# Optimization experiments

Hardware: AMD Instinct MI355X
Metric: run time of the kernel (lower is better)

## Reference

```python
import jax, jax.numpy as jnp
import numpy as np
import itertools

MAX_SRC_PER_MIX = 2
N_OUT = 2 * MAX_SRC_PER_MIX          # 4 estimated sources
N_COMB = 2 ** N_OUT                  # 16 assignment combinations
SNR_MAX = 30.0


def _a_tensor():
    # [16, 2, 4]: row 0 = combination mask, row 1 = its complement
    combos = np.array(list(itertools.product([0, 1], repeat=N_OUT)), dtype=np.float32)
    return jnp.asarray(np.stack([combos, 1.0 - combos], axis=1))


def setup_inputs() -> dict:
    key = jax.random.key(0)
    k1, k2, k3 = jax.random.split(key, 3)
    B, T = 32, 64000
    return {
        "estimated_sources": jax.random.normal(k1, (B, N_OUT, T), dtype=jnp.float32),
        "m1": jax.random.normal(k2, (B, T), dtype=jnp.float32),
        "m2": jax.random.normal(k3, (B, T), dtype=jnp.float32),
    }


def _snr_loss(y, y_pred):
    # y: [K, B, T] estimated mixture, y_pred: [1, B, T] reference mixture
    a = jnp.sum((y - y_pred) ** 2, axis=-1)   # [K, B]
    b = jnp.sum(y ** 2, axis=-1)              # [K, B]
    loss = 10.0 * jnp.log10(a + SNR_MAX * b) - 10.0 * jnp.log10(b)
    return jnp.sum(loss, axis=-1)             # [K]


def reference(estimated_sources, m1, m2):
    A = _a_tensor()                                              # [K, 2, S]
    # all combinations x batch in one contraction (contraction dim S=4)
    mix = jnp.einsum('kcs,bst->kbct', A, estimated_sources)      # [K, B, 2, T]
    losses = _snr_loss(mix[:, :, 0], m1[None]) + _snr_loss(mix[:, :, 1], m2[None])  # [K]
    return jnp.argmin(losses), jnp.min(losses)
```

## Files before the change

### kernel.cpp

```cpp
#include <hip/hip_runtime.h>
#include <math.h>

#define B      32
#define NSRC   4
#define T      64000
#define CH     16
#define NACC   20
#define KCOMB  16
#define TLEN4  ((T / CH) / 4)


__global__ __launch_bounds__(256) void mixit_reduce_kernel(
    const float* __restrict__ est, const float* __restrict__ m1,
    const float* __restrict__ m2, float* __restrict__ ws)
{
    const int b  = blockIdx.x / CH;
    const int ch = blockIdx.x % CH;

    const float4* e0 = (const float4*)(est + (size_t)b * NSRC * T) + (size_t)ch * TLEN4;
    const float4* e1 = e0 + T / 4;
    const float4* e2 = e1 + T / 4;
    const float4* e3 = e2 + T / 4;
    const float4* p1 = (const float4*)(m1 + (size_t)b * T) + (size_t)ch * TLEN4;
    const float4* p2 = (const float4*)(m2 + (size_t)b * T) + (size_t)ch * TLEN4;

    float acc[NACC];
#pragma unroll
    for (int i = 0; i < NACC; i++) acc[i] = 0.0f;

    for (int i = threadIdx.x; i < TLEN4; i += 256) {
        float4 v0 = e0[i], v1 = e1[i], v2 = e2[i], v3 = e3[i];
        float4 w1 = p1[i], w2 = p2[i];
        float A0[4] = {v0.x, v0.y, v0.z, v0.w};
        float A1[4] = {v1.x, v1.y, v1.z, v1.w};
        float A2[4] = {v2.x, v2.y, v2.z, v2.w};
        float A3[4] = {v3.x, v3.y, v3.z, v3.w};
        float M1[4] = {w1.x, w1.y, w1.z, w1.w};
        float M2[4] = {w2.x, w2.y, w2.z, w2.w};
#pragma unroll
        for (int j = 0; j < 4; j++) {
            float s0 = A0[j], s1 = A1[j], s2 = A2[j], s3 = A3[j];
            float x = M1[j], y = M2[j];
            acc[0]  = fmaf(s0, s0, acc[0]);
            acc[1]  = fmaf(s0, s1, acc[1]);
            acc[2]  = fmaf(s0, s2, acc[2]);
            acc[3]  = fmaf(s0, s3, acc[3]);
            acc[4]  = fmaf(s1, s1, acc[4]);
            acc[5]  = fmaf(s1, s2, acc[5]);
            acc[6]  = fmaf(s1, s3, acc[6]);
            acc[7]  = fmaf(s2, s2, acc[7]);
            acc[8]  = fmaf(s2, s3, acc[8]);
            acc[9]  = fmaf(s3, s3, acc[9]);
            acc[10] = fmaf(s0, x,  acc[10]);
            acc[11] = fmaf(s1, x,  acc[11]);
            acc[12] = fmaf(s2, x,  acc[12]);
            acc[13] = fmaf(s3, x,  acc[13]);
            acc[14] = fmaf(s0, y,  acc[14]);
            acc[15] = fmaf(s1, y,  acc[15]);
            acc[16] = fmaf(s2, y,  acc[16]);
            acc[17] = fmaf(s3, y,  acc[17]);
            acc[18] = fmaf(x,  x,  acc[18]);
            acc[19] = fmaf(y,  y,  acc[19]);
        }
    }

#pragma unroll
    for (int i = 0; i < NACC; i++) {
        float v = acc[i];
#pragma unroll
        for (int off = 32; off >= 1; off >>= 1) v += __shfl_xor(v, off, 64);
        acc[i] = v;
    }

    __shared__ float lds[4][NACC];
    const int lane = threadIdx.x & 63;
    const int wave = threadIdx.x >> 6;
    if (lane == 0) {
#pragma unroll
        for (int i = 0; i < NACC; i++) lds[wave][i] = acc[i];
    }
    __syncthreads();
    if (threadIdx.x < NACC) {
        float s = lds[0][threadIdx.x] + lds[1][threadIdx.x] +
                  lds[2][threadIdx.x] + lds[3][threadIdx.x];
        ws[(size_t)blockIdx.x * NACC + threadIdx.x] = s;
    }
}

__global__ __launch_bounds__(256) void mixit_finalize_kernel(
    const float* __restrict__ ws, float* __restrict__ out)
{
    __shared__ float sums[B * NACC];
    __shared__ float losses[KCOMB];

    for (int p = threadIdx.x; p < B * NACC; p += 256) {
        int b = p / NACC, i = p % NACC;
        float s = 0.0f;
        for (int ch = 0; ch < CH; ch++)
            s += ws[(size_t)(b * CH + ch) * NACC + i];
        sums[p] = s;
    }
    __syncthreads();

    if (threadIdx.x < KCOMB) {
        const int k = threadIdx.x;
        float m0 = (float)((k >> 3) & 1);
        float m1b = (float)((k >> 2) & 1);
        float m2b = (float)((k >> 1) & 1);
        float m3 = (float)(k & 1);
        float u0 = 1.0f - m0, u1 = 1.0f - m1b, u2 = 1.0f - m2b, u3 = 1.0f - m3;

        float loss = 0.0f;
        for (int b = 0; b < B; b++) {
            const float* a = sums + b * NACC;
            float g00 = a[0], g01 = a[1], g02 = a[2], g03 = a[3];
            float g11 = a[4], g12 = a[5], g13 = a[6];
            float g22 = a[7], g23 = a[8], g33 = a[9];

            float q0 = m0*m0*g00 + m1b*m1b*g11 + m2b*m2b*g22 + m3*m3*g33
                     + 2.0f*(m0*m1b*g01 + m0*m2b*g02 + m0*m3*g03
                           + m1b*m2b*g12 + m1b*m3*g13 + m2b*m3*g23);
            float q1 = u0*u0*g00 + u1*u1*g11 + u2*u2*g22 + u3*u3*g33
                     + 2.0f*(u0*u1*g01 + u0*u2*g02 + u0*u3*g03
                           + u1*u2*g12 + u1*u3*g13 + u2*u3*g23);
            float d1 = m0*a[10] + m1b*a[11] + m2b*a[12] + m3*a[13];
            float d2 = u0*a[14] + u1*a[15] + u2*a[16] + u3*a[17];
            float n1 = a[18], n2 = a[19];

            float a0 = q0 - 2.0f*d1 + n1;
            float a1 = q1 - 2.0f*d2 + n2;

            loss += 10.0f * (log10f(fmaf(30.0f, q0, a0)) - log10f(q0));
            loss += 10.0f * (log10f(fmaf(30.0f, q1, a1)) - log10f(q1));
        }
        losses[k] = loss;
    }
    __syncthreads();

    if (threadIdx.x == 0) {
        float best = losses[0];
        int bi = 0;
        for (int k = 1; k < KCOMB; k++) {
            if (losses[k] < best) { best = losses[k]; bi = k; }
        }
        out[0] = (float)bi;
        out[1] = best;
    }
}

extern "C" void kernel_launch(void* const* d_in, const int* in_sizes, int n_in,
                              void* d_out, int out_size, void* d_ws, size_t ws_size,
                              hipStream_t stream) {
    const float* est = (const float*)d_in[0];
    const float* m1  = (const float*)d_in[1];
    const float* m2  = (const float*)d_in[2];
    float* ws  = (float*)d_ws;
    float* out = (float*)d_out;

    mixit_reduce_kernel<<<B * CH, 256, 0, stream>>>(est, m1, m2, ws);
    mixit_finalize_kernel<<<1, 256, 0, stream>>>(ws, out);
}
```

Before: 96.59 us.

## Fuse reduce and finalize via last-block atomic counter, add prefetch and DPP reductions

```diff
diff --git a/kernel.cpp b/kernel.cpp
--- a/kernel.cpp
+++ b/kernel.cpp
@@ -7,15 +7,66 @@
 #define CH     16
 #define NACC   20
 #define KCOMB  16
+#define NBLK   (B * CH)
 #define TLEN4  ((T / CH) / 4)
-
-
-__global__ __launch_bounds__(256) void mixit_reduce_kernel(
+#define CNT_BYTE_OFF (NBLK * NACC * 4)
+
+#define DPP_QX1   0xB1
+#define DPP_QX2   0x4E
+#define DPP_HMIRR 0x141
+#define DPP_MIRR  0x140
+
+template <int CTRL>
+__device__ __forceinline__ float dpp_add(float v) {
+    int x = __builtin_amdgcn_update_dpp(0, __float_as_int(v), CTRL, 0xF, 0xF, true);
+    return v + __int_as_float(x);
+}
+
+__device__ __forceinline__ void accum20(float* __restrict__ acc,
+        const float4 v0, const float4 v1, const float4 v2, const float4 v3,
+        const float4 w1, const float4 w2)
+{
+    const float A0[4] = {v0.x, v0.y, v0.z, v0.w};
+    const float A1[4] = {v1.x, v1.y, v1.z, v1.w};
+    const float A2[4] = {v2.x, v2.y, v2.z, v2.w};
+    const float A3[4] = {v3.x, v3.y, v3.z, v3.w};
+    const float M1[4] = {w1.x, w1.y, w1.z, w1.w};
+    const float M2[4] = {w2.x, w2.y, w2.z, w2.w};
+#pragma unroll
+    for (int j = 0; j < 4; j++) {
+        float s0 = A0[j], s1 = A1[j], s2 = A2[j], s3 = A3[j];
+        float x = M1[j], y = M2[j];
+        acc[0]  = fmaf(s0, s0, acc[0]);
+        acc[1]  = fmaf(s0, s1, acc[1]);
+        acc[2]  = fmaf(s0, s2, acc[2]);
+        acc[3]  = fmaf(s0, s3, acc[3]);
+        acc[4]  = fmaf(s1, s1, acc[4]);
+        acc[5]  = fmaf(s1, s2, acc[5]);
+        acc[6]  = fmaf(s1, s3, acc[6]);
+        acc[7]  = fmaf(s2, s2, acc[7]);
+        acc[8]  = fmaf(s2, s3, acc[8]);
+        acc[9]  = fmaf(s3, s3, acc[9]);
+        acc[10] = fmaf(s0, x,  acc[10]);
+        acc[11] = fmaf(s1, x,  acc[11]);
+        acc[12] = fmaf(s2, x,  acc[12]);
+        acc[13] = fmaf(s3, x,  acc[13]);
+        acc[14] = fmaf(s0, y,  acc[14]);
+        acc[15] = fmaf(s1, y,  acc[15]);
+        acc[16] = fmaf(s2, y,  acc[16]);
+        acc[17] = fmaf(s3, y,  acc[17]);
+        acc[18] = fmaf(x,  x,  acc[18]);
+        acc[19] = fmaf(y,  y,  acc[19]);
+    }
+}
+
+__global__ __launch_bounds__(256) void mixit_fused_kernel(
     const float* __restrict__ est, const float* __restrict__ m1,
-    const float* __restrict__ m2, float* __restrict__ ws)
+    const float* __restrict__ m2, float* __restrict__ ws,
+    float* __restrict__ out)
 {
-    const int b  = blockIdx.x / CH;
-    const int ch = blockIdx.x % CH;
+    const int tid = threadIdx.x;
+    const int b   = blockIdx.x / CH;
+    const int ch  = blockIdx.x % CH;
 
     const float4* e0 = (const float4*)(est + (size_t)b * NSRC * T) + (size_t)ch * TLEN4;
     const float4* e1 = e0 + T / 4;
@@ -28,107 +79,100 @@
 #pragma unroll
     for (int i = 0; i < NACC; i++) acc[i] = 0.0f;
 
-    for (int i = threadIdx.x; i < TLEN4; i += 256) {
-        float4 v0 = e0[i], v1 = e1[i], v2 = e2[i], v3 = e3[i];
-        float4 w1 = p1[i], w2 = p2[i];
-        float A0[4] = {v0.x, v0.y, v0.z, v0.w};
-        float A1[4] = {v1.x, v1.y, v1.z, v1.w};
-        float A2[4] = {v2.x, v2.y, v2.z, v2.w};
-        float A3[4] = {v3.x, v3.y, v3.z, v3.w};
-        float M1[4] = {w1.x, w1.y, w1.z, w1.w};
-        float M2[4] = {w2.x, w2.y, w2.z, w2.w};
-#pragma unroll
-        for (int j = 0; j < 4; j++) {
-            float s0 = A0[j], s1 = A1[j], s2 = A2[j], s3 = A3[j];
-            float x = M1[j], y = M2[j];
-            acc[0]  = fmaf(s0, s0, acc[0]);
-            acc[1]  = fmaf(s0, s1, acc[1]);
-            acc[2]  = fmaf(s0, s2, acc[2]);
-            acc[3]  = fmaf(s0, s3, acc[3]);
-            acc[4]  = fmaf(s1, s1, acc[4]);
-            acc[5]  = fmaf(s1, s2, acc[5]);
-            acc[6]  = fmaf(s1, s3, acc[6]);
-            acc[7]  = fmaf(s2, s2, acc[7]);
-            acc[8]  = fmaf(s2, s3, acc[8]);
-            acc[9]  = fmaf(s3, s3, acc[9]);
-            acc[10] = fmaf(s0, x,  acc[10]);
-            acc[11] = fmaf(s1, x,  acc[11]);
-            acc[12] = fmaf(s2, x,  acc[12]);
-            acc[13] = fmaf(s3, x,  acc[13]);
-            acc[14] = fmaf(s0, y,  acc[14]);
-            acc[15] = fmaf(s1, y,  acc[15]);
-            acc[16] = fmaf(s2, y,  acc[16]);
-            acc[17] = fmaf(s3, y,  acc[17]);
-            acc[18] = fmaf(x,  x,  acc[18]);
-            acc[19] = fmaf(y,  y,  acc[19]);
+    int i = tid;
+    float4 c0 = e0[i], c1 = e1[i], c2 = e2[i], c3 = e3[i], c4 = p1[i], c5 = p2[i];
+    while (true) {
+        const int inext = i + 256;
+        const bool hn = inext < TLEN4;
+        float4 n0, n1v, n2v, n3, n4, n5;
+        if (hn) {
+            n0 = e0[inext]; n1v = e1[inext]; n2v = e2[inext];
+            n3 = e3[inext]; n4  = p1[inext]; n5  = p2[inext];
         }
-    }
-
-#pragma unroll
-    for (int i = 0; i < NACC; i++) {
-        float v = acc[i];
-#pragma unroll
-        for (int off = 32; off >= 1; off >>= 1) v += __shfl_xor(v, off, 64);
-        acc[i] = v;
-    }
-
-    __shared__ float lds[4][NACC];
-    const int lane = threadIdx.x & 63;
-    const int wave = threadIdx.x >> 6;
-    if (lane == 0) {
-#pragma unroll
-        for (int i = 0; i < NACC; i++) lds[wave][i] = acc[i];
-    }
-    __syncthreads();
-    if (threadIdx.x < NACC) {
-        float s = lds[0][threadIdx.x] + lds[1][threadIdx.x] +
-                  lds[2][threadIdx.x] + lds[3][threadIdx.x];
-        ws[(size_t)blockIdx.x * NACC + threadIdx.x] = s;
-    }
-}
-
-__global__ __launch_bounds__(256) void mixit_finalize_kernel(
-    const float* __restrict__ ws, float* __restrict__ out)
-{
+        accum20(acc, c0, c1, c2, c3, c4, c5);
+        if (!hn) break;
+        c0 = n0; c1 = n1v; c2 = n2v; c3 = n3; c4 = n4; c5 = n5;
+        i = inext;
+    }
+
+#pragma unroll
+    for (int a = 0; a < NACC; a++) {
+        float v = acc[a];
+        v = dpp_add<DPP_QX1>(v);
+        v = dpp_add<DPP_QX2>(v);
+        v = dpp_add<DPP_HMIRR>(v);
+        v = dpp_add<DPP_MIRR>(v);
+        int x = __builtin_amdgcn_ds_swizzle(__float_as_int(v), 0x401F);
+        acc[a] = v + __int_as_float(x);
+    }
+
+    const int lane = tid & 63;
+    const int wave = tid >> 6;
+    __shared__ float red[8][NACC];
+    if (lane == 0 || lane == 32) {
+        const int r = wave * 2 + (lane >> 5);
+#pragma unroll
+        for (int a = 0; a < NACC; a++) red[r][a] = acc[a];
+    }
+    __syncthreads();
+    if (tid < NACC) {
+        float s = 0.0f;
+#pragma unroll
+        for (int r = 0; r < 8; r++) s += red[r][tid];
+        ws[(size_t)blockIdx.x * NACC + tid] = s;
+    }
+
+    __threadfence();
+    __syncthreads();
+    __shared__ int isLast;
+    if (tid == 0) {
+        unsigned* cnt = (unsigned*)((char*)ws + CNT_BYTE_OFF);
+        unsigned t = __hip_atomic_fetch_add(cnt, 1u, __ATOMIC_ACQ_REL,
+                                            __HIP_MEMORY_SCOPE_AGENT);
+        isLast = (t == NBLK - 1) ? 1 : 0;
+    }
+    __syncthreads();
+    if (!isLast) return;
+    __threadfence();
+
     __shared__ float sums[B * NACC];
+    for (int p = tid; p < B * NACC; p += 256) {
+        const int bb = p / NACC, a = p % NACC;
+        float s = 0.0f;
+#pragma unroll
+        for (int c = 0; c < CH; c++)
+            s += ws[(size_t)(bb * CH + c) * NACC + a];
+        sums[p] = s;
+    }
+    __syncthreads();
+
     __shared__ float losses[KCOMB];
-
-    for (int p = threadIdx.x; p < B * NACC; p += 256) {
-        int b = p / NACC, i = p % NACC;
-        float s = 0.0f;
-        for (int ch = 0; ch < CH; ch++)
-            s += ws[(size_t)(b * CH + ch) * NACC + i];
-        sums[p] = s;
-    }
-    __syncthreads();
-
-    if (threadIdx.x < KCOMB) {
-        const int k = threadIdx.x;
-        float m0 = (float)((k >> 3) & 1);
-        float m1b = (float)((k >> 2) & 1);
-        float m2b = (float)((k >> 1) & 1);
-        float m3 = (float)(k & 1);
-        float u0 = 1.0f - m0, u1 = 1.0f - m1b, u2 = 1.0f - m2b, u3 = 1.0f - m3;
+    if (tid < KCOMB) {
+        const int k = tid;
+        const float k0 = (float)((k >> 3) & 1);
+        const float k1 = (float)((k >> 2) & 1);
+        const float k2 = (float)((k >> 1) & 1);
+        const float k3 = (float)(k & 1);
+        const float u0 = 1.0f - k0, u1 = 1.0f - k1, u2 = 1.0f - k2, u3 = 1.0f - k3;
 
         float loss = 0.0f;
-        for (int b = 0; b < B; b++) {
-            const float* a = sums + b * NACC;
+        for (int bb = 0; bb < B; bb++) {
+            const float* a = sums + bb * NACC;
             float g00 = a[0], g01 = a[1], g02 = a[2], g03 = a[3];
             float g11 = a[4], g12 = a[5], g13 = a[6];
             float g22 = a[7], g23 = a[8], g33 = a[9];
 
-            float q0 = m0*m0*g00 + m1b*m1b*g11 + m2b*m2b*g22 + m3*m3*g33
-                     + 2.0f*(m0*m1b*g01 + m0*m2b*g02 + m0*m3*g03
-                           + m1b*m2b*g12 + m1b*m3*g13 + m2b*m3*g23);
+            float q0 = k0*k0*g00 + k1*k1*g11 + k2*k2*g22 + k3*k3*g33
+                     + 2.0f*(k0*k1*g01 + k0*k2*g02 + k0*k3*g03
+                           + k1*k2*g12 + k1*k3*g13 + k2*k3*g23);
             float q1 = u0*u0*g00 + u1*u1*g11 + u2*u2*g22 + u3*u3*g33
                      + 2.0f*(u0*u1*g01 + u0*u2*g02 + u0*u3*g03
                            + u1*u2*g12 + u1*u3*g13 + u2*u3*g23);
-            float d1 = m0*a[10] + m1b*a[11] + m2b*a[12] + m3*a[13];
+            float d1 = k0*a[10] + k1*a[11] + k2*a[12] + k3*a[13];
             float d2 = u0*a[14] + u1*a[15] + u2*a[16] + u3*a[17];
-            float n1 = a[18], n2 = a[19];
-
-            float a0 = q0 - 2.0f*d1 + n1;
-            float a1 = q1 - 2.0f*d2 + n2;
+
+            float a0 = q0 - 2.0f*d1 + a[18];
+            float a1 = q1 - 2.0f*d2 + a[19];
 
             loss += 10.0f * (log10f(fmaf(30.0f, q0, a0)) - log10f(q0));
             loss += 10.0f * (log10f(fmaf(30.0f, q1, a1)) - log10f(q1));
@@ -137,12 +181,11 @@
     }
     __syncthreads();
 
-    if (threadIdx.x == 0) {
+    if (tid == 0) {
         float best = losses[0];
         int bi = 0;
-        for (int k = 1; k < KCOMB; k++) {
+        for (int k = 1; k < KCOMB; k++)
             if (losses[k] < best) { best = losses[k]; bi = k; }
-        }
         out[0] = (float)bi;
         out[1] = best;
     }
@@ -157,6 +200,6 @@
     float* ws  = (float*)d_ws;
     float* out = (float*)d_out;
 
-    mixit_reduce_kernel<<<B * CH, 256, 0, stream>>>(est, m1, m2, ws);
-    mixit_finalize_kernel<<<1, 256, 0, stream>>>(ws, out);
-}
+    (void)hipMemsetAsync((char*)d_ws + CNT_BYTE_OFF, 0, 4, stream);
+    mixit_fused_kernel<<<NBLK, 256, 0, stream>>>(est, m1, m2, ws, out);
+}
```

Result: slower. 132.7 us (+37.4%).
